# Kernel tuning notes

Hardware: AMD Instinct MI355X
Metric: run time of the kernel (lower is better)

The kernel has to match this reference:

```python
import jax, jax.numpy as jnp
import numpy as np

B, N, D, H = 512, 129, 256, 8   # batch, nodes (128 customers + depot), d_model, heads
HD = D // H                      # head_depth = 32
T = 128                          # decode steps
CLIP = 10.0                      # tanh_clipping
CAP = 1.0                        # VRPproblem.VEHICLE_CAPACITY


def setup_inputs() -> dict:
    key = jax.random.key(0)
    ks = jax.random.split(key, 9)
    s = 1.0 / np.sqrt(D)  # dense-layer init scale, keeps tanh logits unsaturated
    return {
        "embeddings": jax.random.normal(ks[0], (B, N, D), jnp.float32),
        "context_vectors": jax.random.normal(ks[1], (B, D), jnp.float32),
        "demands": jax.random.uniform(ks[2], (B, N), jnp.float32) * 0.1,
        "Wq_context": jax.random.normal(ks[3], (D, D), jnp.float32) * s,
        "Wq_step": jax.random.normal(ks[4], (D + 1, D), jnp.float32) * s,
        "Wk": jax.random.normal(ks[5], (D, D), jnp.float32) * s,
        "Wk_tanh": jax.random.normal(ks[6], (D, D), jnp.float32) * s,
        "Wv": jax.random.normal(ks[7], (D, D), jnp.float32) * s,
        "Wo": jax.random.normal(ks[8], (D, D), jnp.float32) * s,
    }


def _decode(embeddings, context_vectors, demands, Wq_context, Wq_step, Wk, Wk_tanh, Wv, Wo):
    b, n, dm = embeddings.shape
    hd = dm // H
    neg_inf = jnp.float32(-jnp.inf)
    # Precomputed once per rollout (as in the original call())
    K = (embeddings @ Wk).reshape(b, n, H, hd).transpose(0, 2, 1, 3)    # [b,H,n,hd]
    V = (embeddings @ Wv).reshape(b, n, H, hd).transpose(0, 2, 1, 3)    # [b,H,n,hd]
    Kt = embeddings @ Wk_tanh                                            # [b,n,dm]
    Qc = context_vectors @ Wq_context                                    # [b,dm]
    node_ids = jnp.arange(n)

    def step(carry, _):
        prev, used, visited = carry  # [b] int32, [b] f32, [b,n] bool (True = masked)
        # get_step_context: gather prev-node embedding, append remaining capacity
        cur = jnp.take_along_axis(embeddings, prev[:, None, None], axis=1)[:, 0]  # [b,dm]
        ctx = jnp.concatenate([cur, CAP - used[:, None]], axis=-1)                # [b,dm+1]
        Q = (Qc + ctx @ Wq_step).reshape(b, H, hd)                                # split heads, seq=1
        # decoder_mha: note original divides by head_depth (not sqrt)
        compat = jnp.einsum('bhd,bhnd->bhn', Q, K) / jnp.float32(hd)
        compat = jnp.where(visited[:, None, :], neg_inf, compat)
        attn = jnp.einsum('bhn,bhnd->bhd', jax.nn.softmax(compat, axis=-1), V)
        glimpse = attn.reshape(b, dm) @ Wo                                        # w_out
        # get_log_p: tanh-clipped pointer logits over all nodes
        logits = jnp.tanh(jnp.einsum('bd,bnd->bn', glimpse, Kt) / jnp.sqrt(jnp.float32(dm))) * CLIP
        logits = jnp.where(visited, neg_inf, logits)
        log_p = jax.nn.log_softmax(logits, axis=-1)                               # [b,n]
        # greedy _select_node + clip to valid range
        sel = jnp.clip(jnp.argmax(log_p, axis=-1).astype(jnp.int32), 0, n - 1)
        # state.step: visit node (depot index 0 always stays feasible), capacity update
        dem = jnp.take_along_axis(demands, sel[:, None], axis=1)[:, 0]
        used2 = jnp.where(sel == 0, jnp.float32(0.0), used + dem)
        visited2 = jnp.where(node_ids[None, :] == sel[:, None], sel[:, None] != 0, visited)
        return (sel, used2, visited2), (log_p, sel)

    init = (jnp.zeros((b,), jnp.int32), jnp.zeros((b,), jnp.float32), jnp.zeros((b, n), bool))
    _, (lp, pi) = jax.lax.scan(step, init, None, length=T)
    return lp.transpose(1, 0, 2), pi.T  # [b,T,n], [b,T]


def reference(embeddings, context_vectors, demands, Wq_context, Wq_step, Wk, Wk_tanh, Wv, Wo):
    log_probs, pi = _decode(embeddings, context_vectors, demands,
                            Wq_context, Wq_step, Wk, Wk_tanh, Wv, Wo)
    return log_probs, pi.astype(jnp.float32)
```

## Files before the change

### kernel.cpp

```cpp
#include <hip/hip_runtime.h>
#include <math.h>

#define NB 512
#define NN 129
#define DMM 256
#define NH 8
#define HDm 32
#define TT 128

#define PI_OFF ((size_t)NB * TT * NN)

#define NEG_SENTINEL (-1.0e30f)

#define EQ_SZ ((size_t)NB * NN * DMM)
#define V_OFF (EQ_SZ)
#define W2_OFF (2 * EQ_SZ)
#define QC_OFF (2 * EQ_SZ + (size_t)DMM * DMM)

__device__ __forceinline__ float tanh_fast(float x) {
  return 1.0f - 2.0f / (__expf(2.0f * x) + 1.0f);
}

__global__ __launch_bounds__(256) void w2_kernel(const float* __restrict__ Wkt,
                                                 const float* __restrict__ Wo,
                                                 float* __restrict__ W2) {
  __shared__ __align__(16) float rowL[DMM];
  int d = blockIdx.x, i = threadIdx.x;
  rowL[i] = Wkt[d * DMM + i];
  __syncthreads();
  const float4* wo4 = (const float4*)(Wo + (size_t)i * DMM);
  const float4* r4 = (const float4*)rowL;
  float acc = 0.f;
  #pragma unroll 8
  for (int jq = 0; jq < DMM / 4; ++jq) {
    float4 a = r4[jq], bq = wo4[jq];
    acc += a.x * bq.x + a.y * bq.y + a.z * bq.z + a.w * bq.w;
  }
  W2[d * DMM + i] = acc;
}

__global__ __launch_bounds__(256) void qc_kernel(const float* __restrict__ ctx,
                                                 const float* __restrict__ Wqc,
                                                 float* __restrict__ Qc) {
  __shared__ __align__(16) float cL[DMM];
  int b = blockIdx.x, j = threadIdx.x;
  cL[j] = ctx[b * DMM + j];
  __syncthreads();
  float acc = 0.f;
  for (int i = 0; i < DMM; ++i) acc += cL[i] * Wqc[i * DMM + j];
  Qc[b * DMM + j] = acc;
}

__global__ __launch_bounds__(256) void eqv_kernel(const float* __restrict__ emb,
                                                  const float* __restrict__ Wqs,
                                                  const float* __restrict__ Wv,
                                                  float* __restrict__ Eq,
                                                  float* __restrict__ Vws) {
  __shared__ __align__(16) float eL[64][DMM];
  int j = threadIdx.x;
  size_t r0 = (size_t)blockIdx.x * 64;
  for (int k = 0; k < 64; ++k) eL[k][j] = emb[(r0 + k) * DMM + j];
  __syncthreads();
  float accE[64], accV[64];
  #pragma unroll
  for (int r = 0; r < 64; ++r) { accE[r] = 0.f; accV[r] = 0.f; }
  for (int iq = 0; iq < 64; ++iq) {
    float we[4], wv[4];
    #pragma unroll
    for (int k = 0; k < 4; ++k) {
      we[k] = Wqs[(iq * 4 + k) * DMM + j];
      wv[k] = Wv[(iq * 4 + k) * DMM + j];
    }
    #pragma unroll
    for (int r = 0; r < 64; ++r) {
      float4 e = *(const float4*)&eL[r][iq * 4];
      accE[r] += e.x * we[0] + e.y * we[1] + e.z * we[2] + e.w * we[3];
      accV[r] += e.x * wv[0] + e.y * wv[1] + e.z * wv[2] + e.w * wv[3];
    }
  }
  for (int r = 0; r < 64; ++r) {
    Eq[(r0 + r) * DMM + j] = accE[r];
    Vws[(r0 + r) * DMM + j] = accV[r];
  }
}

__global__ __launch_bounds__(512, 2) void decode_kernel(
    const float* __restrict__ emb, const float* __restrict__ demands,
    const float* __restrict__ Wk, const float* __restrict__ Wqs,
    const float* __restrict__ Eq, const float* __restrict__ W2,
    const float* __restrict__ Qc, const float* __restrict__ Vws,
    float* __restrict__ out) {
  extern __shared__ float sm[];
  float* K128L = sm;
  float* T128L = sm + 256;
  float* V128L = sm + 512;
  float* demL = sm + 768;
  float* SCR = sm + 904;
  float* SCR2 = SCR + 33156;
  float* embL = SCR;
  float* WkT = SCR2;
  float* W2T = SCR2 + 2048;
  float* EqL = SCR;
  float* qL = SCR2;
  float* pm = SCR2 + 256;
  float* attnL = SCR2 + 1312;
  float* ypd = SCR2 + 1568;

  const int tid = threadIdx.x;
  const int b = blockIdx.x;
  const int w = tid >> 6;
  const int l = tid & 63;
  const int dv = l & 31, h2 = l >> 5;

  const float* embB = emb + (size_t)b * NN * DMM;

  for (int idx = tid; idx < NN * DMM; idx += 512) {
    int r = idx >> 8, c = idx & 255;
    embL[r * 257 + c] = embB[idx];
  }
  if (tid < 132) demL[tid] = (tid < NN) ? demands[b * NN + tid] : 0.f;
  __syncthreads();

  if (tid < 256) {
    float a0 = 0.f, a1 = 0.f;
    for (int i = 0; i < DMM; ++i) {
      float e = embL[128 * 257 + i];
      a0 += e * Wk[i * DMM + tid];
      a1 += e * W2[i * DMM + tid];
    }
    K128L[tid] = a0;
    T128L[tid] = a1;
    V128L[tid] = Vws[((size_t)b * NN + 128) * DMM + tid];
  }

  float Kr0[HDm], Kr1[HDm], Tr0[HDm], Tr1[HDm];
  #pragma unroll
  for (int d = 0; d < HDm; ++d) { Kr0[d] = 0.f; Kr1[d] = 0.f; Tr0[d] = 0.f; Tr1[d] = 0.f; }
  for (int it = 0; it < 32; ++it) {
    __syncthreads();
    for (int idx = tid; idx < 2048; idx += 512) {
      WkT[idx] = Wk[it * 2048 + idx];
      W2T[idx] = W2[it * 2048 + idx];
    }
    __syncthreads();
    for (int i = 0; i < 8; ++i) {
      float e0 = embL[l * 257 + it * 8 + i];
      float e1 = embL[(l + 64) * 257 + it * 8 + i];
      const float4* wk4 = (const float4*)(WkT + i * DMM + w * HDm);
      const float4* w24 = (const float4*)(W2T + i * DMM + w * HDm);
      #pragma unroll
      for (int c = 0; c < 8; ++c) {
        float4 kv = wk4[c], tv = w24[c];
        Kr0[4*c+0] += e0 * kv.x; Kr0[4*c+1] += e0 * kv.y; Kr0[4*c+2] += e0 * kv.z; Kr0[4*c+3] += e0 * kv.w;
        Kr1[4*c+0] += e1 * kv.x; Kr1[4*c+1] += e1 * kv.y; Kr1[4*c+2] += e1 * kv.z; Kr1[4*c+3] += e1 * kv.w;
        Tr0[4*c+0] += e0 * tv.x; Tr0[4*c+1] += e0 * tv.y; Tr0[4*c+2] += e0 * tv.z; Tr0[4*c+3] += e0 * tv.w;
        Tr1[4*c+0] += e1 * tv.x; Tr1[4*c+1] += e1 * tv.y; Tr1[4*c+2] += e1 * tv.z; Tr1[4*c+3] += e1 * tv.w;
      }
    }
  }

  float Vr[64];
  {
    const float* vb = Vws + ((size_t)b * NN + h2 * 64) * DMM + w * HDm + dv;
    #pragma unroll
    for (int jj = 0; jj < 64; ++jj) Vr[jj] = vb[(size_t)jj * DMM];
  }

  float qcR = Qc[b * DMM + w * HDm + dv];
  float wqR = Wqs[256 * DMM + w * HDm + dv];
  float eqR = Eq[((size_t)b * NN + 0) * DMM + w * HDm + dv];

  __syncthreads();
  {
    const float* EqB = Eq + (size_t)b * NN * DMM;
    for (int idx = tid; idx < NN * DMM; idx += 512) {
      int r = idx >> 8, c = idx & 255;
      EqL[r * 257 + c] = EqB[idx];
    }
  }

  float used = 0.f;
  int vis0 = 0, vis1 = 0, vis128 = 0;
  __syncthreads();

  float* outB = out + (size_t)b * TT * NN;

  for (int t = 0; t < TT; ++t) {
    float qd = qcR + eqR + (1.0f - used) * wqR;
    if (l < 32) qL[w * HDm + l] = qd;

    float s0, s1, s2;
    {
      const float4* q4 = (const float4*)(qL + w * HDm);
      const float4* k4 = (const float4*)(K128L + w * HDm);
      float a0 = 0.f, a1 = 0.f, a2 = 0.f, a3 = 0.f;
      float b0 = 0.f, b1 = 0.f, b2 = 0.f, b3 = 0.f;
      float c0 = 0.f, c1 = 0.f, c2 = 0.f, c3 = 0.f;
      #pragma unroll
      for (int c = 0; c < 8; ++c) {
        float4 q = q4[c], k = k4[c];
        a0 += q.x * Kr0[4*c];   a1 += q.y * Kr0[4*c+1];
        a2 += q.z * Kr0[4*c+2]; a3 += q.w * Kr0[4*c+3];
        b0 += q.x * Kr1[4*c];   b1 += q.y * Kr1[4*c+1];
        b2 += q.z * Kr1[4*c+2]; b3 += q.w * Kr1[4*c+3];
        c0 += q.x * k.x; c1 += q.y * k.y; c2 += q.z * k.z; c3 += q.w * k.w;
      }
      s0 = ((a0 + a1) + (a2 + a3)) * 0.03125f;
      s1 = ((b0 + b1) + (b2 + b3)) * 0.03125f;
      s2 = ((c0 + c1) + (c2 + c3)) * 0.03125f;
    }
    if (vis0) s0 = -INFINITY;
    if (vis1) s1 = -INFINITY;
    float e0 = __expf(s0), e1 = __expf(s1);
    float e2 = (l == 0 && !vis128) ? __expf(s2) : 0.f;
    pm[w * 132 + l] = e0;
    pm[w * 132 + 64 + l] = e1;
    if (l == 0) pm[w * 132 + 128] = e2;
    float psum = e0 + e1 + e2;

    float acc;
    {
      const float4* pr = (const float4*)(pm + w * 132 + h2 * 64);
      float a0 = 0.f, a1 = 0.f, a2 = 0.f, a3 = 0.f;
      #pragma unroll
      for (int jq = 0; jq < 16; ++jq) {
        float4 p4 = pr[jq];
        a0 += p4.x * Vr[4*jq];   a1 += p4.y * Vr[4*jq+1];
        a2 += p4.z * Vr[4*jq+2]; a3 += p4.w * Vr[4*jq+3];
      }
      acc = (a0 + a1) + (a2 + a3);
    }
    if (h2 == 0) acc += pm[w * 132 + 128] * V128L[w * HDm + dv];
    #pragma unroll
    for (int o = 32; o > 0; o >>= 1) psum += __shfl_xor(psum, o);
    acc += __shfl_xor(acc, 32);
    acc *= (1.0f / psum);
    if (l < 32) attnL[w * HDm + l] = acc;

    float* ypb = ypd + (t & 1) * 1056;
    float y0, y1;
    {
      const float4* a4 = (const float4*)(attnL + w * HDm);
      float a0 = 0.f, a1 = 0.f, a2 = 0.f, a3 = 0.f;
      float b0 = 0.f, b1 = 0.f, b2 = 0.f, b3 = 0.f;
      #pragma unroll
      for (int c = 0; c < 8; ++c) {
        float4 a = a4[c];
        a0 += a.x * Tr0[4*c];   a1 += a.y * Tr0[4*c+1];
        a2 += a.z * Tr0[4*c+2]; a3 += a.w * Tr0[4*c+3];
        b0 += a.x * Tr1[4*c];   b1 += a.y * Tr1[4*c+1];
        b2 += a.z * Tr1[4*c+2]; b3 += a.w * Tr1[4*c+3];
      }
      y0 = (a0 + a1) + (a2 + a3);
      y1 = (b0 + b1) + (b2 + b3);
    }
    ypb[w * 132 + l] = y0;
    ypb[w * 132 + 64 + l] = y1;
    {
      float yy = 0.f;
      if (l < 8) {
        float4 a = ((const float4*)(attnL + w * HDm))[l];
        float4 tq = ((const float4*)(T128L + w * HDm))[l];
        yy = a.x * tq.x + a.y * tq.y + a.z * tq.z + a.w * tq.w;
      }
      yy += __shfl_xor(yy, 4);
      yy += __shfl_xor(yy, 2);
      yy += __shfl_xor(yy, 1);
      if (l == 0) ypb[w * 132 + 128] = yy;
    }

    __syncthreads();

    const float* yp = ypd + (t & 1) * 1056;
    float ya = 0.f, yb = 0.f, ys = 0.f;
    #pragma unroll
    for (int ww = 0; ww < 8; ++ww) {
      ya += yp[ww * 132 + l];
      yb += yp[ww * 132 + 64 + l];
      ys += yp[ww * 132 + 128];
    }
    float ra = vis0 ? -INFINITY : ya;
    float rb = vis1 ? -INFINITY : yb;
    float rc = (l == 0 && !vis128) ? ys : -INFINITY;

    float bv = ra;
    int bi = l;
    if (rb > bv) { bv = rb; bi = l + 64; }
    if (rc > bv) { bv = rc; bi = 128; }
    #pragma unroll
    for (int o = 32; o > 0; o >>= 1) {
      float ov = __shfl_xor(bv, o);
      int oi = __shfl_xor(bi, o);
      if (ov > bv || (ov == bv && oi < bi)) { bv = ov; bi = oi; }
    }
    const int sel = bi;
    float eqNew = EqL[sel * 257 + w * HDm + dv];
    float dmv = demL[sel];

    if (w == 0) {
      float ta = vis0 ? -INFINITY : 10.f * tanh_fast(ya * 0.0625f);
      float tb = vis1 ? -INFINITY : 10.f * tanh_fast(yb * 0.0625f);
      float tc = (l == 0 && !vis128) ? 10.f * tanh_fast(ys * 0.0625f) : -INFINITY;
      float ea = __expf(ta), eb = __expf(tb);
      float ec = (l == 0 && !vis128) ? __expf(tc) : 0.f;
      float se = ea + eb + ec;
      #pragma unroll
      for (int o = 32; o > 0; o >>= 1) se += __shfl_xor(se, o);
      float lse = __logf(se);
      float* op = outB + (size_t)t * NN;
      op[l] = fmaxf(ta - lse, NEG_SENTINEL);
      op[l + 64] = fmaxf(tb - lse, NEG_SENTINEL);
      if (l == 0) {
        op[128] = fmaxf(tc - lse, NEG_SENTINEL);
        out[PI_OFF + (size_t)b * TT + t] = (float)sel;
      }
    }

    used = (sel == 0) ? 0.f : used + dmv;
    if (sel == l && sel != 0) vis0 = 1;
    if (sel == l + 64) vis1 = 1;
    if (sel == 128) vis128 = 1;
    eqR = eqNew;
  }
}

extern "C" void kernel_launch(void* const* d_in, const int* in_sizes, int n_in,
                              void* d_out, int out_size, void* d_ws, size_t ws_size,
                              hipStream_t stream) {
  const float* emb = (const float*)d_in[0];
  const float* ctx = (const float*)d_in[1];
  const float* dem = (const float*)d_in[2];
  const float* Wqc = (const float*)d_in[3];
  const float* Wqs = (const float*)d_in[4];
  const float* Wk = (const float*)d_in[5];
  const float* Wkt = (const float*)d_in[6];
  const float* Wv = (const float*)d_in[7];
  const float* Wo = (const float*)d_in[8];
  float* out = (float*)d_out;
  float* ws = (float*)d_ws;

  float* Eq = ws;
  float* Vws = ws + V_OFF;
  float* W2 = ws + W2_OFF;
  float* Qc = ws + QC_OFF;

  w2_kernel<<<dim3(DMM), dim3(DMM), 0, stream>>>(Wkt, Wo, W2);
  qc_kernel<<<dim3(NB), dim3(DMM), 0, stream>>>(ctx, Wqc, Qc);
  eqv_kernel<<<dim3((NB * NN) / 64), dim3(256), 0, stream>>>(emb, Wqs, Wv, Eq, Vws);

  const int SMEM = 38156 * 4;
  hipFuncSetAttribute(reinterpret_cast<const void*>(decode_kernel),
                      hipFuncAttributeMaxDynamicSharedMemorySize, SMEM);
  decode_kernel<<<dim3(NB), dim3(512), SMEM, stream>>>(emb, dem, Wk, Wqs, Eq, W2, Qc,
                                                       Vws, out);
}
```

Measured before the change: 1.417 ms.

## Defer log-softmax output to next step, distribute stores, use ballot argmax

```diff
diff --git a/kernel.cpp b/kernel.cpp
--- a/kernel.cpp
+++ b/kernel.cpp
@@ -100,7 +100,6 @@
   float* embL = SCR;
   float* WkT = SCR2;
   float* W2T = SCR2 + 2048;
-  float* EqL = SCR;
   float* qL = SCR2;
   float* pm = SCR2 + 256;
   float* attnL = SCR2 + 1312;
@@ -170,17 +169,9 @@
   float wqR = Wqs[256 * DMM + w * HDm + dv];
   float eqR = Eq[((size_t)b * NN + 0) * DMM + w * HDm + dv];
 
-  __syncthreads();
-  {
-    const float* EqB = Eq + (size_t)b * NN * DMM;
-    for (int idx = tid; idx < NN * DMM; idx += 512) {
-      int r = idx >> 8, c = idx & 255;
-      EqL[r * 257 + c] = EqB[idx];
-    }
-  }
-
   float used = 0.f;
   int vis0 = 0, vis1 = 0, vis128 = 0;
+  float pa = 0.f, pb = 0.f, pc = 0.f;
   __syncthreads();
 
   float* outB = out + (size_t)b * TT * NN;
@@ -188,6 +179,26 @@
   for (int t = 0; t < TT; ++t) {
     float qd = qcR + eqR + (1.0f - used) * wqR;
     if (l < 32) qL[w * HDm + l] = qd;
+
+    if (t > 0) {
+      float ta = (pa == -INFINITY) ? -INFINITY : 10.f * tanh_fast(pa * 0.0625f);
+      float tb = (pb == -INFINITY) ? -INFINITY : 10.f * tanh_fast(pb * 0.0625f);
+      float tc = (l == 0 && pc != -INFINITY) ? 10.f * tanh_fast(pc * 0.0625f)
+                                             : -INFINITY;
+      float ea = __expf(ta), eb = __expf(tb);
+      float ec = (l == 0) ? __expf(tc) : 0.f;
+      float se = ea + eb + ec;
+      #pragma unroll
+      for (int o = 32; o > 0; o >>= 1) se += __shfl_xor(se, o);
+      float lse = __logf(se);
+      float* op = outB + (size_t)(t - 1) * NN;
+      if (w < 4) {
+        if ((l >> 4) == w) op[l] = fmaxf(ta - lse, NEG_SENTINEL);
+      } else {
+        if ((l >> 4) == w - 4) op[l + 64] = fmaxf(tb - lse, NEG_SENTINEL);
+      }
+      if (w == 0 && l == 0) op[128] = fmaxf(tc - lse, NEG_SENTINEL);
+    }
 
     float s0, s1, s2;
     {
@@ -231,11 +242,11 @@
       acc = (a0 + a1) + (a2 + a3);
     }
     if (h2 == 0) acc += pm[w * 132 + 128] * V128L[w * HDm + dv];
+    acc += __shfl_xor(acc, 32);
+    if (l < 32) attnL[w * HDm + l] = acc;
     #pragma unroll
     for (int o = 32; o > 0; o >>= 1) psum += __shfl_xor(psum, o);
-    acc += __shfl_xor(acc, 32);
-    acc *= (1.0f / psum);
-    if (l < 32) attnL[w * HDm + l] = acc;
+    float inv = 1.0f / psum;
 
     float* ypb = ypd + (t & 1) * 1056;
     float y0, y1;
@@ -251,8 +262,8 @@
         b0 += a.x * Tr1[4*c];   b1 += a.y * Tr1[4*c+1];
         b2 += a.z * Tr1[4*c+2]; b3 += a.w * Tr1[4*c+3];
       }
-      y0 = (a0 + a1) + (a2 + a3);
-      y1 = (b0 + b1) + (b2 + b3);
+      y0 = ((a0 + a1) + (a2 + a3)) * inv;
+      y1 = ((b0 + b1) + (b2 + b3)) * inv;
     }
     ypb[w * 132 + l] = y0;
     ypb[w * 132 + 64 + l] = y1;
@@ -266,7 +277,7 @@
       yy += __shfl_xor(yy, 4);
       yy += __shfl_xor(yy, 2);
       yy += __shfl_xor(yy, 1);
-      if (l == 0) ypb[w * 132 + 128] = yy;
+      if (l == 0) ypb[w * 132 + 128] = yy * inv;
     }
 
     __syncthreads();
@@ -283,44 +294,45 @@
     float rb = vis1 ? -INFINITY : yb;
     float rc = (l == 0 && !vis128) ? ys : -INFINITY;
 
-    float bv = ra;
-    int bi = l;
-    if (rb > bv) { bv = rb; bi = l + 64; }
-    if (rc > bv) { bv = rc; bi = 128; }
-    #pragma unroll
-    for (int o = 32; o > 0; o >>= 1) {
-      float ov = __shfl_xor(bv, o);
-      int oi = __shfl_xor(bi, o);
-      if (ov > bv || (ov == bv && oi < bi)) { bv = ov; bi = oi; }
-    }
-    const int sel = bi;
-    float eqNew = EqL[sel * 257 + w * HDm + dv];
+    float mx = fmaxf(fmaxf(ra, rb), rc);
+    #pragma unroll
+    for (int o = 32; o > 0; o >>= 1) mx = fmaxf(mx, __shfl_xor(mx, o));
+    unsigned long long ba = __ballot(ra == mx);
+    unsigned long long bb = __ballot(rb == mx);
+    int sel = ba ? (__ffsll((long long)ba) - 1)
+                 : (bb ? 64 + (__ffsll((long long)bb) - 1) : 128);
+
+    float eqNew = Eq[((size_t)b * NN + sel) * DMM + w * HDm + dv];
     float dmv = demL[sel];
-
-    if (w == 0) {
-      float ta = vis0 ? -INFINITY : 10.f * tanh_fast(ya * 0.0625f);
-      float tb = vis1 ? -INFINITY : 10.f * tanh_fast(yb * 0.0625f);
-      float tc = (l == 0 && !vis128) ? 10.f * tanh_fast(ys * 0.0625f) : -INFINITY;
-      float ea = __expf(ta), eb = __expf(tb);
-      float ec = (l == 0 && !vis128) ? __expf(tc) : 0.f;
-      float se = ea + eb + ec;
-      #pragma unroll
-      for (int o = 32; o > 0; o >>= 1) se += __shfl_xor(se, o);
-      float lse = __logf(se);
-      float* op = outB + (size_t)t * NN;
-      op[l] = fmaxf(ta - lse, NEG_SENTINEL);
-      op[l + 64] = fmaxf(tb - lse, NEG_SENTINEL);
-      if (l == 0) {
-        op[128] = fmaxf(tc - lse, NEG_SENTINEL);
-        out[PI_OFF + (size_t)b * TT + t] = (float)sel;
-      }
-    }
+    if (w == 0 && l == 0) out[PI_OFF + (size_t)b * TT + t] = (float)sel;
+
+    pa = ra; pb = rb; pc = rc;
 
     used = (sel == 0) ? 0.f : used + dmv;
     if (sel == l && sel != 0) vis0 = 1;
     if (sel == l + 64) vis1 = 1;
     if (sel == 128) vis128 = 1;
     eqR = eqNew;
+  }
+
+  {
+    float ta = (pa == -INFINITY) ? -INFINITY : 10.f * tanh_fast(pa * 0.0625f);
+    float tb = (pb == -INFINITY) ? -INFINITY : 10.f * tanh_fast(pb * 0.0625f);
+    float tc = (l == 0 && pc != -INFINITY) ? 10.f * tanh_fast(pc * 0.0625f)
+                                           : -INFINITY;
+    float ea = __expf(ta), eb = __expf(tb);
+    float ec = (l == 0) ? __expf(tc) : 0.f;
+    float se = ea + eb + ec;
+    #pragma unroll
+    for (int o = 32; o > 0; o >>= 1) se += __shfl_xor(se, o);
+    float lse = __logf(se);
+    float* op = outB + (size_t)(TT - 1) * NN;
+    if (w < 4) {
+      if ((l >> 4) == w) op[l] = fmaxf(ta - lse, NEG_SENTINEL);
+    } else {
+      if ((l >> 4) == w - 4) op[l + 64] = fmaxf(tb - lse, NEG_SENTINEL);
+    }
+    if (w == 0 && l == 0) op[128] = fmaxf(tc - lse, NEG_SENTINEL);
   }
 }
 
```

Result: faster. 1.354 ms (median of 2 runs) (-4.5%).
